# Kernel tuning notes

Measured on AMD Instinct MI355X. Metric: run time of the kernel, lower is better.

The kernel has to match this reference:

```python
import jax, jax.numpy as jnp
import numpy as np
from jax import lax

EPS = 1e-5

# ---- 1-bit activation quantizer with straight-through estimator ----
@jax.custom_vjp
def ste_sign(x):
    return jnp.sign(x)

def _ste_sign_fwd(x):
    return jnp.sign(x), x

def _ste_sign_bwd(res, g):
    x = res
    # clipped STE: pass gradient where |x| <= 1
    return (g * (jnp.abs(x) <= 1.0).astype(g.dtype),)

ste_sign.defvjp(_ste_sign_fwd, _ste_sign_bwd)

# ---- 1-bit weight binarization: sign(w) * per-out-channel mean(|w|), STE ----
@jax.custom_vjp
def bin_weight(w):
    alpha = jnp.mean(jnp.abs(w), axis=(1, 2, 3), keepdims=True)  # [O,1,1,1]
    return jnp.sign(w) * alpha

def _bw_fwd(w):
    return bin_weight(w), w

def _bw_bwd(res, g):
    w = res
    # weight_clip=1: straight-through inside the clip range
    return (g * (jnp.abs(w) <= 1.0).astype(g.dtype),)

bin_weight.defvjp(_bw_fwd, _bw_bwd)

def conv3x3(x, w):
    # zero padding=1, stride=1, NCHW / OIHW
    return lax.conv_general_dilated(
        x, w, window_strides=(1, 1), padding=((1, 1), (1, 1)),
        dimension_numbers=('NCHW', 'OIHW', 'NCHW'))

def batchnorm(x, gamma, beta):
    # training-mode BN with batch statistics over (N,H,W)
    mean = jnp.mean(x, axis=(0, 2, 3), keepdims=True)
    var = jnp.var(x, axis=(0, 2, 3), keepdims=True)
    xn = (x - mean) * lax.rsqrt(var + EPS)
    return xn * gamma[None, :, None, None] + beta[None, :, None, None]


def setup_inputs() -> dict:
    key = jax.random.key(0)
    k1, k2, k3 = jax.random.split(key, 3)
    N, C, H, W = 32, 256, 56, 56
    return {
        'x': jax.random.normal(k1, (N, C, H, W), dtype=jnp.float32),
        'w1': jax.random.normal(k2, (C, C, 3, 3), dtype=jnp.float32) * 0.05,
        'gamma1': jnp.ones((C,), dtype=jnp.float32),
        'beta1': jnp.zeros((C,), dtype=jnp.float32),
        'w2': jax.random.normal(k3, (C, C, 3, 3), dtype=jnp.float32) * 0.05,
        'gamma2': jnp.ones((C,), dtype=jnp.float32),
        'beta2': jnp.zeros((C,), dtype=jnp.float32),
    }


def reference(x, w1, gamma1, beta1, w2, gamma2, beta2):
    identity = x
    out = ste_sign(x)                       # quantized activation (1-bit, signed)
    out = conv3x3(out, bin_weight(w1))      # BinConv 3x3, stride 1
    out = batchnorm(out, gamma1, beta1)
    out = ste_sign(out)
    out = conv3x3(out, bin_weight(w2))
    out = batchnorm(out, gamma2, beta2)
    return out + identity                   # residual add (downsample=None)
```

## Files before the change

kernel.cpp:

```cpp
#include <hip/hip_runtime.h>
#include <stdint.h>

#define NB 32
#define CH 256
#define HH 56
#define WW 56
#define HWSZ (HH*WW)
#define NPIX (NB*HWSZ)
#define HP 58
#define WP 58
#define PADPIX (NB*HP*WP)
#define NTAPS 9
#define KKE (CH*NTAPS)
#define NPIXD 100352.0
#define WQ_CONV (NTAPS*8*8*64*16)
#define HSTRIDE 272

typedef int int4v  __attribute__((ext_vector_type(4)));
typedef int int16v __attribute__((ext_vector_type(16)));
typedef unsigned int uint4v __attribute__((ext_vector_type(4)));

__global__ void init_kernel(long long* __restrict__ sums8) {
    int t = blockIdx.x*256 + threadIdx.x;
    if (t < 2*8*512) sums8[t] = 0;
}

__global__ void wqpack_kernel(const float* __restrict__ w1, const float* __restrict__ w2,
                              int8_t* __restrict__ wq) {
    int t = blockIdx.x*256 + threadIdx.x;
    int conv = blockIdx.y;
    const float* w = conv ? w2 : w1;
    int lane = t & 63;
    int g = t >> 6;
    int nb = g & 7, h = g >> 3;
    int ks = h & 7, tap = h >> 3;
    int o = nb*32 + (lane & 31);
    int cin0 = ks*32 + (lane >> 5)*16;
    int wd[4];
    #pragma unroll
    for (int q = 0; q < 4; ++q) {
        int wv = 0;
        #pragma unroll
        for (int j = 0; j < 4; ++j) {
            float v = w[(size_t)(o*CH + cin0 + q*4 + j)*NTAPS + tap];
            int s = (v > 0.f) ? 1 : ((v < 0.f) ? -1 : 0);
            wv |= (s & 0xff) << (8*j);
        }
        wd[q] = wv;
    }
    *(int4v*)(wq + (size_t)conv*WQ_CONV + (size_t)t*16) = (int4v){wd[0], wd[1], wd[2], wd[3]};
}

__global__ void alpha_kernel(const float* __restrict__ w1, const float* __restrict__ w2,
                             float* __restrict__ alpha) {
    int o = blockIdx.x; int conv = blockIdx.y;
    const float* w = conv ? w2 : w1;
    float s = 0.f;
    for (int i = threadIdx.x; i < KKE; i += 256) s += fabsf(w[(size_t)o*KKE + i]);
    for (int off = 32; off; off >>= 1) s += __shfl_down(s, off);
    __shared__ float l[4];
    int lane = threadIdx.x & 63, wv = threadIdx.x >> 6;
    if (lane == 0) l[wv] = s;
    __syncthreads();
    if (threadIdx.x == 0) alpha[conv*CH + o] = (l[0]+l[1]+l[2]+l[3]) * (1.f/KKE);
}

__global__ void pack_x_kernel(const float* __restrict__ x, int8_t* __restrict__ apad) {
    int p = blockIdx.x*256 + threadIdx.x;
    if (p >= PADPIX) return;
    int n  = p / (HP*WP);
    int r  = p - n*(HP*WP);
    int hp = r / WP, wp = r - hp*WP;
    int4v* dst = (int4v*)(apad + (size_t)p*CH);
    if (hp >= 1 && hp <= HH && wp >= 1 && wp <= WW) {
        const float* xb = x + (size_t)n*CH*HWSZ + (hp-1)*WW + (wp-1);
        #pragma unroll 2
        for (int c16 = 0; c16 < 16; ++c16) {
            int wd[4];
            #pragma unroll
            for (int q = 0; q < 4; ++q) {
                int wv = 0;
                #pragma unroll
                for (int j = 0; j < 4; ++j) {
                    float v = xb[(size_t)(c16*16 + q*4 + j)*HWSZ];
                    int s = (v > 0.f) ? 1 : ((v < 0.f) ? -1 : 0);
                    wv |= (s & 0xff) << (8*j);
                }
                wd[q] = wv;
            }
            dst[c16] = (int4v){wd[0], wd[1], wd[2], wd[3]};
        }
    } else {
        int4v z = {0,0,0,0};
        #pragma unroll
        for (int c16 = 0; c16 < 16; ++c16) dst[c16] = z;
    }
}

#define ISSUE_SET(IT) do { \
        int k_ = (IT) % 3; \
        int tap_ = (IT) >> 3; \
        int toff_ = (tap_/3)*10 + (tap_ - (tap_/3)*3); \
        int ch_ = 2*((IT) & 7) + kh; \
        int pr0_ = pix0 + toff_; \
        int pr1_ = pr0_ + 40; \
        uint32_t ad0_ = halob + (uint32_t)(pr0_*HSTRIDE + ((ch_ ^ ((pr0_>>3)&7)) << 4)); \
        uint32_t ad1_ = halob + (uint32_t)(pr1_*HSTRIDE + ((ch_ ^ ((pr1_>>3)&7)) << 4)); \
        uint32_t vo_ = voff + (uint32_t)(IT)*8192u; \
        asm volatile("ds_read_b128 %0, %1" : "=v"(as_[k_][0]) : "v"(ad0_)); \
        asm volatile("ds_read_b128 %0, %1" : "=v"(as_[k_][1]) : "v"(ad1_)); \
        asm volatile("buffer_load_dwordx4 %0, %1, %2, 0 offen" \
                     : "=v"(bs_[k_][0]) : "v"(vo_), "s"(rsrc)); \
        asm volatile("buffer_load_dwordx4 %0, %1, %2, 0 offen offset:1024" \
                     : "=v"(bs_[k_][1]) : "v"(vo_), "s"(rsrc)); \
    } while (0)

#define CONV_BODY \
    __syncthreads(); \
    int lane = t & 63; \
    int nbp = __builtin_amdgcn_readfirstlane(t >> 6); \
    int kh = lane >> 5, lr = lane & 31; \
    int r0 = lr >> 3, c0 = lr & 7; \
    int pix0 = r0*10 + c0; \
    uint32_t halob = (uint32_t)(uintptr_t)halo; \
    uint32_t voff = (uint32_t)(nbp*2048 + lane*16); \
    uint4v rsrc; \
    { union { const int8_t* p; unsigned long long u; } pu_; pu_.p = wq; \
      rsrc.x = (unsigned)pu_.u; rsrc.y = (unsigned)(pu_.u >> 32); \
      rsrc.z = 0xffffffffu; rsrc.w = 0x00020000u; } \
    int4v as_[3][2], bs_[3][2]; \
    int16v acc00, acc01, acc10, acc11; \
    _Pragma("unroll") \
    for (int i = 0; i < 16; ++i) { acc00[i]=0; acc01[i]=0; acc10[i]=0; acc11[i]=0; } \
    ISSUE_SET(0); \
    ISSUE_SET(1); \
    _Pragma("unroll") \
    for (int it = 0; it < 72; ++it) { \
        if (it + 1 < 72) { asm volatile("s_waitcnt lgkmcnt(2) vmcnt(2)"); } \
        else             { asm volatile("s_waitcnt lgkmcnt(0) vmcnt(0)"); } \
        __builtin_amdgcn_sched_barrier(0); \
        if (it + 2 < 72) { ISSUE_SET(it + 2); } \
        int kc_ = it % 3; \
        acc00 = __builtin_amdgcn_mfma_i32_32x32x32_i8(as_[kc_][0], bs_[kc_][0], acc00, 0,0,0); \
        acc01 = __builtin_amdgcn_mfma_i32_32x32x32_i8(as_[kc_][0], bs_[kc_][1], acc01, 0,0,0); \
        acc10 = __builtin_amdgcn_mfma_i32_32x32x32_i8(as_[kc_][1], bs_[kc_][0], acc10, 0,0,0); \
        acc11 = __builtin_amdgcn_mfma_i32_32x32x32_i8(as_[kc_][1], bs_[kc_][1], acc11, 0,0,0); \
    } \
    { \
        int s1a = 0, s2a = 0, s1b = 0, s2b = 0; \
        _Pragma("unroll") \
        for (int reg = 0; reg < 16; ++reg) { \
            int row_ = (reg & 3) + 8*(reg >> 2) + 4*kh; \
            _Pragma("unroll") \
            for (int m = 0; m < 2; ++m) { \
                int pm_ = m*32 + row_; \
                int rr_ = pm_ >> 3, cc_ = pm_ & 7; \
                size_t pbase_ = (size_t)((n0*HH + ty*8 + rr_)*WW + tx*8 + cc_)*CH; \
                int v0 = (m ? acc10[reg] : acc00[reg]); \
                int v1 = (m ? acc11[reg] : acc01[reg]); \
                cnt[pbase_ + (nbp*2+0)*32 + lr] = (int16_t)v0; \
                cnt[pbase_ + (nbp*2+1)*32 + lr] = (int16_t)v1; \
                s1a += v0; s2a += v0*v0; s1b += v1; s2b += v1*v1; \
            } \
        } \
        s1a += __shfl_down(s1a, 32); s2a += __shfl_down(s2a, 32); \
        s1b += __shfl_down(s1b, 32); s2b += __shfl_down(s2b, 32); \
        if (lane < 32) { \
            long long* sp = sums8 + (size_t)(b & 7)*512; \
            int ch0 = nbp*64 + lr, ch1 = ch0 + 32; \
            atomicAdd((unsigned long long*)&sp[2*ch0],   (unsigned long long)(long long)s1a); \
            atomicAdd((unsigned long long*)&sp[2*ch0+1], (unsigned long long)(long long)s2a); \
            atomicAdd((unsigned long long*)&sp[2*ch1],   (unsigned long long)(long long)s1b); \
            atomicAdd((unsigned long long*)&sp[2*ch1+1], (unsigned long long)(long long)s2b); \
        } \
    }

__global__ __launch_bounds__(256, 4) void conv_kernel(
        const int8_t* __restrict__ apad, const int8_t* __restrict__ wq,
        int16_t* __restrict__ cnt, long long* __restrict__ sums8) {
    __shared__ __attribute__((aligned(16))) int8_t halo[100*HSTRIDE];
    int b = blockIdx.x;
    int tile = b % 49, n0 = b / 49;
    int ty = tile / 7, tx = tile % 7;
    int t = threadIdx.x;

    #pragma unroll 1
    for (int j = 0; j < 7; ++j) {
        int idx = t + j*256;
        if (idx < 1600) {
            int pix = idx >> 4, c16 = idx & 15;
            int dr = pix / 10, dc = pix - dr*10;
            const int4v* src = (const int4v*)(apad +
                ((size_t)((n0*HP + ty*8+dr)*WP + tx*8+dc))*CH + c16*16);
            *(int4v*)&halo[pix*HSTRIDE + ((c16 ^ ((pix >> 3) & 7)) << 4)] = *src;
        }
    }
    CONV_BODY
}

__global__ __launch_bounds__(256, 4) void conv2_kernel(
        const int16_t* __restrict__ src16, const float* __restrict__ ab,
        const int8_t* __restrict__ wq,
        int16_t* __restrict__ cnt, long long* __restrict__ sums8) {
    __shared__ __attribute__((aligned(16))) int8_t halo[100*HSTRIDE];
    int b = blockIdx.x;
    int tile = b % 49, n0 = b / 49;
    int ty = tile / 7, tx = tile % 7;
    int t = threadIdx.x;

    {
        int c16s = t & 15;
        #pragma unroll 1
        for (int k = 0; k < 7; ++k) {
            int pix = (t >> 4) + k*16;
            if (pix < 100) {
                int dr = pix / 10, dc = pix - dr*10;
                int hi = ty*8 + dr - 1, wi = tx*8 + dc - 1;
                int4v outv = {0,0,0,0};
                if ((unsigned)hi < (unsigned)HH && (unsigned)wi < (unsigned)WW) {
                    const int16_t* sp = src16 + ((size_t)(n0*HH + hi)*WW + wi)*CH + c16s*16;
                    int4v u0 = *(const int4v*)sp;
                    int4v u1 = *(const int4v*)(sp + 8);
                    int wd[4];
                    #pragma unroll
                    for (int q = 0; q < 4; ++q) {
                        int wv = 0;
                        #pragma unroll
                        for (int j = 0; j < 4; ++j) {
                            int e = q*4 + j;
                            int word = (e < 8) ? u0[e >> 1] : u1[(e-8) >> 1];
                            int sval = (e & 1) ? (word >> 16) : ((word << 16) >> 16);
                            int ch = c16s*16 + e;
                            float v = fmaf(ab[ch], (float)sval, ab[CH + ch]);
                            int s = (v > 0.f) ? 1 : ((v < 0.f) ? -1 : 0);
                            wv |= (s & 0xff) << (8*j);
                        }
                        wd[q] = wv;
                    }
                    outv = (int4v){wd[0], wd[1], wd[2], wd[3]};
                }
                *(int4v*)&halo[pix*HSTRIDE + ((c16s ^ ((pix >> 3) & 7)) << 4)] = outv;
            }
        }
    }
    CONV_BODY
}

__global__ void bncoef_kernel(const long long* __restrict__ sums8,
                              const float* __restrict__ alpha,
                              const float* __restrict__ gamma, const float* __restrict__ beta,
                              float* __restrict__ ab) {
    int o = threadIdx.x;
    long long S1i = 0, S2i = 0;
    #pragma unroll
    for (int k = 0; k < 8; ++k) {
        S1i += sums8[(size_t)k*512 + 2*o];
        S2i += sums8[(size_t)k*512 + 2*o + 1];
    }
    double S1 = (double)S1i, S2 = (double)S2i;
    double mean = S1 / NPIXD;
    double var  = S2 / NPIXD - mean*mean;
    double al   = (double)alpha[o];
    double rs   = 1.0 / sqrt(al*al*var + 1e-5);
    double a    = (double)gamma[o] * al * rs;
    ab[o]      = (float)a;
    ab[CH + o] = (float)((double)beta[o] - a*mean);
}

__global__ __launch_bounds__(256) void final_kernel(const int16_t* __restrict__ cnt,
        const float* __restrict__ x, const float* __restrict__ ab, float* __restrict__ out) {
    __shared__ int4v lsd4[64*32];
    int8_t* lb = (int8_t*)lsd4;
    int b = blockIdx.x;
    int n = b / 49, tile = b - n*49;
    int p0 = tile * 64;
    int t = threadIdx.x;
    const int4v* src = (const int4v*)(cnt + ((size_t)n*HWSZ + p0)*CH);
    #pragma unroll
    for (int j = 0; j < 8; ++j) {
        int c = t + j*256;
        int pix = c >> 5, c16 = c & 31;
        *(int4v*)&lb[pix*512 + ((c16*16) ^ ((pix & 15) << 4))] = src[c];
    }
    __syncthreads();
    int pixL = t & 63;
    int cb = (t >> 6) * 64;
    #pragma unroll 1
    for (int i = 0; i < 8; ++i) {
        int ch0 = cb + i*8;
        int4v v = *(const int4v*)&lb[pixL*512 + ((ch0*2) ^ ((pixL & 15) << 4))];
        #pragma unroll
        for (int j = 0; j < 8; ++j) {
            int ch = ch0 + j;
            int word = v[j >> 1];
            int sval = (j & 1) ? (word >> 16) : ((word << 16) >> 16);
            size_t g = (size_t)(n*CH + ch)*HWSZ + p0 + pixL;
            out[g] = fmaf(ab[ch], (float)sval, ab[CH + ch]) + x[g];
        }
    }
}

extern "C" void kernel_launch(void* const* d_in, const int* in_sizes, int n_in,
                              void* d_out, int out_size, void* d_ws, size_t ws_size,
                              hipStream_t stream) {
    const float* x  = (const float*)d_in[0];
    const float* w1 = (const float*)d_in[1];
    const float* g1 = (const float*)d_in[2];
    const float* b1 = (const float*)d_in[3];
    const float* w2 = (const float*)d_in[4];
    const float* g2 = (const float*)d_in[5];
    const float* b2 = (const float*)d_in[6];
    float* out = (float*)d_out;

    char* ws = (char*)d_ws;
    size_t off = 0;
    auto alloc = [&](size_t nbytes) { char* pp = ws + off; off = (off + nbytes + 255) & ~(size_t)255; return pp; };
    int8_t*   apad  = (int8_t*)alloc((size_t)PADPIX*CH);
    int16_t*  cnt1  = (int16_t*)alloc((size_t)NPIX*CH*2);
    int16_t*  cnt2  = (int16_t*)alloc((size_t)NPIX*CH*2);
    int8_t*   wq    = (int8_t*)alloc((size_t)2*WQ_CONV);
    float*    alpha = (float*)alloc((size_t)2*CH*4);
    long long* sums8 = (long long*)alloc((size_t)2*8*512*8);
    float*    ab    = (float*)alloc((size_t)2*2*CH*4);

    init_kernel<<<32, 256, 0, stream>>>(sums8);
    wqpack_kernel<<<dim3(144, 2), 256, 0, stream>>>(w1, w2, wq);
    alpha_kernel<<<dim3(CH, 2), 256, 0, stream>>>(w1, w2, alpha);
    pack_x_kernel<<<(PADPIX + 255)/256, 256, 0, stream>>>(x, apad);

    conv_kernel<<<1568, 256, 0, stream>>>(apad, wq, cnt1, sums8);
    bncoef_kernel<<<1, CH, 0, stream>>>(sums8, alpha, g1, b1, ab);

    conv2_kernel<<<1568, 256, 0, stream>>>(cnt1, ab, wq + WQ_CONV, cnt2, sums8 + 8*512);
    bncoef_kernel<<<1, CH, 0, stream>>>(sums8 + 8*512, alpha + CH, g2, b2, ab + 2*CH);

    final_kernel<<<1568, 256, 0, stream>>>(cnt2, x, ab + 2*CH, out);
}
```

Before: 238.0 us.

## Process two images per conv block to reuse weight loads across 128 pixels

Each conv block now covers the same 8x8 spatial tile for two batch images. It loads a 200-pixel halo and issues eight MFMAs per k-step instead of four, so every global weight load feeds twice as many pixels. The grid is halved, launch bounds drop from 4 to 2 blocks per CU, and LDS and accumulator registers double. The trade-off is lower occupancy and fewer blocks (784) to fill the device, in exchange for less global weight traffic per output.

New measurement: 239.7 us. No clear change (+0.7%).

```diff
diff --git a/kernel.cpp b/kernel.cpp
--- a/kernel.cpp
+++ b/kernel.cpp
@@ -102,13 +102,19 @@
         int tap_ = (IT) >> 3; \
         int toff_ = (tap_/3)*10 + (tap_ - (tap_/3)*3); \
         int ch_ = 2*((IT) & 7) + kh; \
-        int pr0_ = pix0 + toff_; \
-        int pr1_ = pr0_ + 40; \
-        uint32_t ad0_ = halob + (uint32_t)(pr0_*HSTRIDE + ((ch_ ^ ((pr0_>>3)&7)) << 4)); \
-        uint32_t ad1_ = halob + (uint32_t)(pr1_*HSTRIDE + ((ch_ ^ ((pr1_>>3)&7)) << 4)); \
+        int p0_ = pix0 + toff_; \
+        int p1_ = p0_ + 40; \
+        int p2_ = p0_ + 100; \
+        int p3_ = p1_ + 100; \
+        uint32_t ad0_ = halob + (uint32_t)(p0_*HSTRIDE + ((ch_ ^ ((p0_>>3)&7)) << 4)); \
+        uint32_t ad1_ = halob + (uint32_t)(p1_*HSTRIDE + ((ch_ ^ ((p1_>>3)&7)) << 4)); \
+        uint32_t ad2_ = halob + (uint32_t)(p2_*HSTRIDE + ((ch_ ^ ((p2_>>3)&7)) << 4)); \
+        uint32_t ad3_ = halob + (uint32_t)(p3_*HSTRIDE + ((ch_ ^ ((p3_>>3)&7)) << 4)); \
         uint32_t vo_ = voff + (uint32_t)(IT)*8192u; \
         asm volatile("ds_read_b128 %0, %1" : "=v"(as_[k_][0]) : "v"(ad0_)); \
         asm volatile("ds_read_b128 %0, %1" : "=v"(as_[k_][1]) : "v"(ad1_)); \
+        asm volatile("ds_read_b128 %0, %1" : "=v"(as_[k_][2]) : "v"(ad2_)); \
+        asm volatile("ds_read_b128 %0, %1" : "=v"(as_[k_][3]) : "v"(ad3_)); \
         asm volatile("buffer_load_dwordx4 %0, %1, %2, 0 offen" \
                      : "=v"(bs_[k_][0]) : "v"(vo_), "s"(rsrc)); \
         asm volatile("buffer_load_dwordx4 %0, %1, %2, 0 offen offset:1024" \
@@ -128,15 +134,18 @@
     { union { const int8_t* p; unsigned long long u; } pu_; pu_.p = wq; \
       rsrc.x = (unsigned)pu_.u; rsrc.y = (unsigned)(pu_.u >> 32); \
       rsrc.z = 0xffffffffu; rsrc.w = 0x00020000u; } \
-    int4v as_[3][2], bs_[3][2]; \
-    int16v acc00, acc01, acc10, acc11; \
+    int4v as_[3][4], bs_[3][2]; \
+    int16v acc00, acc01, acc10, acc11, acc20, acc21, acc30, acc31; \
     _Pragma("unroll") \
-    for (int i = 0; i < 16; ++i) { acc00[i]=0; acc01[i]=0; acc10[i]=0; acc11[i]=0; } \
+    for (int i = 0; i < 16; ++i) { \
+        acc00[i]=0; acc01[i]=0; acc10[i]=0; acc11[i]=0; \
+        acc20[i]=0; acc21[i]=0; acc30[i]=0; acc31[i]=0; \
+    } \
     ISSUE_SET(0); \
     ISSUE_SET(1); \
     _Pragma("unroll") \
     for (int it = 0; it < 72; ++it) { \
-        if (it + 1 < 72) { asm volatile("s_waitcnt lgkmcnt(2) vmcnt(2)"); } \
+        if (it + 1 < 72) { asm volatile("s_waitcnt lgkmcnt(4) vmcnt(2)"); } \
         else             { asm volatile("s_waitcnt lgkmcnt(0) vmcnt(0)"); } \
         __builtin_amdgcn_sched_barrier(0); \
         if (it + 2 < 72) { ISSUE_SET(it + 2); } \
@@ -145,6 +154,10 @@
         acc01 = __builtin_amdgcn_mfma_i32_32x32x32_i8(as_[kc_][0], bs_[kc_][1], acc01, 0,0,0); \
         acc10 = __builtin_amdgcn_mfma_i32_32x32x32_i8(as_[kc_][1], bs_[kc_][0], acc10, 0,0,0); \
         acc11 = __builtin_amdgcn_mfma_i32_32x32x32_i8(as_[kc_][1], bs_[kc_][1], acc11, 0,0,0); \
+        acc20 = __builtin_amdgcn_mfma_i32_32x32x32_i8(as_[kc_][2], bs_[kc_][0], acc20, 0,0,0); \
+        acc21 = __builtin_amdgcn_mfma_i32_32x32x32_i8(as_[kc_][2], bs_[kc_][1], acc21, 0,0,0); \
+        acc30 = __builtin_amdgcn_mfma_i32_32x32x32_i8(as_[kc_][3], bs_[kc_][0], acc30, 0,0,0); \
+        acc31 = __builtin_amdgcn_mfma_i32_32x32x32_i8(as_[kc_][3], bs_[kc_][1], acc31, 0,0,0); \
     } \
     { \
         int s1a = 0, s2a = 0, s1b = 0, s2b = 0; \
@@ -152,12 +165,16 @@
         for (int reg = 0; reg < 16; ++reg) { \
             int row_ = (reg & 3) + 8*(reg >> 2) + 4*kh; \
             _Pragma("unroll") \
-            for (int m = 0; m < 2; ++m) { \
-                int pm_ = m*32 + row_; \
+            for (int mm = 0; mm < 4; ++mm) { \
+                int img_ = mm >> 1; \
+                int pm_ = (mm & 1)*32 + row_; \
                 int rr_ = pm_ >> 3, cc_ = pm_ & 7; \
-                size_t pbase_ = (size_t)((n0*HH + ty*8 + rr_)*WW + tx*8 + cc_)*CH; \
-                int v0 = (m ? acc10[reg] : acc00[reg]); \
-                int v1 = (m ? acc11[reg] : acc01[reg]); \
+                size_t pbase_ = (size_t)(((n0+img_)*HH + ty*8 + rr_)*WW + tx*8 + cc_)*CH; \
+                int v0, v1; \
+                if (mm == 0)      { v0 = acc00[reg]; v1 = acc01[reg]; } \
+                else if (mm == 1) { v0 = acc10[reg]; v1 = acc11[reg]; } \
+                else if (mm == 2) { v0 = acc20[reg]; v1 = acc21[reg]; } \
+                else              { v0 = acc30[reg]; v1 = acc31[reg]; } \
                 cnt[pbase_ + (nbp*2+0)*32 + lr] = (int16_t)v0; \
                 cnt[pbase_ + (nbp*2+1)*32 + lr] = (int16_t)v1; \
                 s1a += v0; s2a += v0*v0; s1b += v1; s2b += v1*v1; \
@@ -175,50 +192,56 @@
         } \
     }
 
-__global__ __launch_bounds__(256, 4) void conv_kernel(
+__global__ __launch_bounds__(256, 2) void conv_kernel(
         const int8_t* __restrict__ apad, const int8_t* __restrict__ wq,
         int16_t* __restrict__ cnt, long long* __restrict__ sums8) {
-    __shared__ __attribute__((aligned(16))) int8_t halo[100*HSTRIDE];
+    __shared__ __attribute__((aligned(16))) int8_t halo[200*HSTRIDE];
     int b = blockIdx.x;
-    int tile = b % 49, n0 = b / 49;
+    int tile = b % 49, npair = b / 49;
     int ty = tile / 7, tx = tile % 7;
+    int n0 = npair * 2;
     int t = threadIdx.x;
 
     #pragma unroll 1
-    for (int j = 0; j < 7; ++j) {
+    for (int j = 0; j < 13; ++j) {
         int idx = t + j*256;
-        if (idx < 1600) {
+        if (idx < 3200) {
             int pix = idx >> 4, c16 = idx & 15;
-            int dr = pix / 10, dc = pix - dr*10;
+            int img = (pix >= 100) ? 1 : 0;
+            int hp = pix - img*100;
+            int dr = hp / 10, dc = hp - dr*10;
             const int4v* src = (const int4v*)(apad +
-                ((size_t)((n0*HP + ty*8+dr)*WP + tx*8+dc))*CH + c16*16);
+                ((size_t)(((n0+img)*HP + ty*8+dr)*WP + tx*8+dc))*CH + c16*16);
             *(int4v*)&halo[pix*HSTRIDE + ((c16 ^ ((pix >> 3) & 7)) << 4)] = *src;
         }
     }
     CONV_BODY
 }
 
-__global__ __launch_bounds__(256, 4) void conv2_kernel(
+__global__ __launch_bounds__(256, 2) void conv2_kernel(
         const int16_t* __restrict__ src16, const float* __restrict__ ab,
         const int8_t* __restrict__ wq,
         int16_t* __restrict__ cnt, long long* __restrict__ sums8) {
-    __shared__ __attribute__((aligned(16))) int8_t halo[100*HSTRIDE];
+    __shared__ __attribute__((aligned(16))) int8_t halo[200*HSTRIDE];
     int b = blockIdx.x;
-    int tile = b % 49, n0 = b / 49;
+    int tile = b % 49, npair = b / 49;
     int ty = tile / 7, tx = tile % 7;
+    int n0 = npair * 2;
     int t = threadIdx.x;
 
     {
         int c16s = t & 15;
         #pragma unroll 1
-        for (int k = 0; k < 7; ++k) {
+        for (int k = 0; k < 13; ++k) {
             int pix = (t >> 4) + k*16;
-            if (pix < 100) {
-                int dr = pix / 10, dc = pix - dr*10;
+            if (pix < 200) {
+                int img = (pix >= 100) ? 1 : 0;
+                int hp = pix - img*100;
+                int dr = hp / 10, dc = hp - dr*10;
                 int hi = ty*8 + dr - 1, wi = tx*8 + dc - 1;
                 int4v outv = {0,0,0,0};
                 if ((unsigned)hi < (unsigned)HH && (unsigned)wi < (unsigned)WW) {
-                    const int16_t* sp = src16 + ((size_t)(n0*HH + hi)*WW + wi)*CH + c16s*16;
+                    const int16_t* sp = src16 + ((size_t)((n0+img)*HH + hi)*WW + wi)*CH + c16s*16;
                     int4v u0 = *(const int4v*)sp;
                     int4v u1 = *(const int4v*)(sp + 8);
                     int wd[4];
@@ -328,10 +351,10 @@
     alpha_kernel<<<dim3(CH, 2), 256, 0, stream>>>(w1, w2, alpha);
     pack_x_kernel<<<(PADPIX + 255)/256, 256, 0, stream>>>(x, apad);
 
-    conv_kernel<<<1568, 256, 0, stream>>>(apad, wq, cnt1, sums8);
+    conv_kernel<<<784, 256, 0, stream>>>(apad, wq, cnt1, sums8);
     bncoef_kernel<<<1, CH, 0, stream>>>(sums8, alpha, g1, b1, ab);
 
-    conv2_kernel<<<1568, 256, 0, stream>>>(cnt1, ab, wq + WQ_CONV, cnt2, sums8 + 8*512);
+    conv2_kernel<<<784, 256, 0, stream>>>(cnt1, ab, wq + WQ_CONV, cnt2, sums8 + 8*512);
     bncoef_kernel<<<1, CH, 0, stream>>>(sums8 + 8*512, alpha + CH, g2, b2, ab + 2*CH);
 
     final_kernel<<<1568, 256, 0, stream>>>(cnt2, x, ab + 2*CH, out);
```
